# Optimization experiments

Measured on AMD Instinct MI355X. Metric: run time of the kernel, lower is better.

The kernel has to match this reference:

```python
import jax, jax.numpy as jnp
import numpy as np

# 9 jitter shifts: (L, R, T, B) padding applied to `input`; `target` gets the
# opposite padding (L<->R, T<->B swapped), producing a 1-pixel relative shift.
SHIFTS = ((0, 0, 0, 0), (0, 0, 1, 0), (0, 0, 0, 1), (1, 0, 0, 0), (0, 1, 0, 0),
          (1, 0, 1, 0), (0, 1, 0, 1), (0, 1, 1, 0), (1, 0, 0, 1))
SMIN_K = 32.0


def _shifted_diff(inp, tgt, L, R, T, B):
    # get_opposite in the original simply swaps the pad pair
    Lt, Rt = R, L
    Tt, Bt = B, T
    # ConstantPad2d((L,R,T,B)) pads last dim by (L,R), second-to-last by (T,B)
    pi = jnp.pad(inp, ((0, 0), (T, B), (L, R)))
    pt = jnp.pad(tgt, ((0, 0), (Tt, Bt), (Lt, Rt)))  # same padded shape
    d = jnp.abs(pi - pt)
    n, m, k = d.shape
    # crop back to the original (batch, max_len, dim) window
    return d[:, T:m - B, L:k - R]


def setup_inputs() -> dict:
    key = jax.random.key(0)
    k1, k2 = jax.random.split(key)
    B, T, D = 64, 2048, 80
    return {
        "input": jax.random.normal(k1, (B, T, D), dtype=jnp.float32),
        "target": jax.random.normal(k2, (B, T, D), dtype=jnp.float32),
    }


def reference(input, target):
    # (batch, max_len, dim, 9): abs-diff for each of the 9 relative shifts
    diffs = jnp.stack(
        [_shifted_diff(input, target, L, R, T, B) for (L, R, T, B) in SHIFTS],
        axis=-1,
    )
    # smooth minimum over the 9 shifts: -log(sum(exp(-k*t)))/k (stable via logsumexp)
    sm = -jax.scipy.special.logsumexp(-SMIN_K * diffs, axis=-1) / SMIN_K
    center = diffs[..., 0]  # unshifted abs-diff
    # average of the center diff and the smooth-min, reduced to a scalar loss
    return 0.5 * (jnp.mean(center) + jnp.mean(sm))
```

## Files before the change

### kernel.cpp

```cpp
#include <hip/hip_runtime.h>
#include <math.h>

#define BATCH 64
#define TLEN 2048
#define DIM 80
#define DQ (DIM / 4)
#define TT 8
#define TCHUNKS (TLEN / TT)
#define THREADS 256
#define NSTRIPS (BATCH * TCHUNKS * DQ)
#define NBLOCKS (NSTRIPS / THREADS)

#define SMIN_C  46.166241308446828f
#define SMIN_RC 0.02166084939249829f

__device__ __forceinline__ void load_row(float r[6], const float* __restrict__ base,
                                         int t, int q) {
    if (t >= 0 && t < TLEN) {
        const float* p = base + (size_t)t * DIM;
        const float4 v = *(const float4*)p;
        r[0] = (q > 0)      ? p[-1] : 0.f;
        r[1] = v.x; r[2] = v.y; r[3] = v.z; r[4] = v.w;
        r[5] = (q < DQ - 1) ? p[4]  : 0.f;
    } else {
#pragma unroll
        for (int i = 0; i < 6; ++i) r[i] = 0.f;
    }
}

__device__ __forceinline__ float elem_loss(float x, const float* rm, const float* r0,
                                           const float* rp, int e) {
    float v[9];
#pragma unroll
    for (int i = 0; i < 3; ++i) {
        v[0 + i] = fabsf(x - rm[e + i]);
        v[3 + i] = fabsf(x - r0[e + i]);
        v[6 + i] = fabsf(x - rp[e + i]);
    }
    const float center = v[4];
    float m = fminf(fminf(fminf(v[0], v[1]), fminf(v[2], v[3])),
                    fminf(fminf(v[4], v[5]), fminf(v[6], v[7])));
    m = fminf(m, v[8]);
    float S = 0.f;
#pragma unroll
    for (int s = 0; s < 9; ++s)
        S += __builtin_amdgcn_exp2f(SMIN_C * (m - v[s]));
    const float sm = m - __builtin_amdgcn_logf(S) * SMIN_RC;
    return center + sm;
}

__global__ __launch_bounds__(THREADS) void jitter_kernel(
    const float* __restrict__ inp, const float* __restrict__ tgt,
    float* __restrict__ ws)
{
    __shared__ float wsum[THREADS / 64];

    const int n   = blockIdx.x * THREADS + threadIdx.x;
    const int q   = n % DQ;
    const int rem = n / DQ;
    const int tc  = rem % TCHUNKS;
    const int b   = rem / TCHUNKS;
    const int t0  = tc * TT;
    const int d0  = q * 4;

    const float* tgb = tgt + (size_t)b * TLEN * DIM + d0;
    const float* inb = inp + (size_t)b * TLEN * DIM + d0;

    float rm[6], r0[6], rp[6];
    load_row(rm, tgb, t0 - 1, q);
    load_row(r0, tgb, t0,     q);

    float acc = 0.f;
#pragma unroll
    for (int lt = 0; lt < TT; ++lt) {
        load_row(rp, tgb, t0 + lt + 1, q);
        const float4 in4 = *(const float4*)(inb + (size_t)(t0 + lt) * DIM);
        acc += elem_loss(in4.x, rm, r0, rp, 0);
        acc += elem_loss(in4.y, rm, r0, rp, 1);
        acc += elem_loss(in4.z, rm, r0, rp, 2);
        acc += elem_loss(in4.w, rm, r0, rp, 3);
#pragma unroll
        for (int i = 0; i < 6; ++i) { rm[i] = r0[i]; r0[i] = rp[i]; }
    }

#pragma unroll
    for (int off = 32; off > 0; off >>= 1)
        acc += __shfl_down(acc, off, 64);
    const int lane = threadIdx.x & 63, wid = threadIdx.x >> 6;
    if (lane == 0) wsum[wid] = acc;
    __syncthreads();
    if (threadIdx.x == 0) {
        float tot = 0.f;
#pragma unroll
        for (int w = 0; w < THREADS / 64; ++w) tot += wsum[w];
        ws[blockIdx.x] = tot;
    }
}

__global__ __launch_bounds__(256) void reduce_kernel(const float* __restrict__ ws,
                                                     float* __restrict__ out) {
    __shared__ float wsum[4];
    float s = 0.f;
    for (int i = threadIdx.x; i < NBLOCKS; i += 256) s += ws[i];
#pragma unroll
    for (int off = 32; off > 0; off >>= 1)
        s += __shfl_down(s, off, 64);
    const int lane = threadIdx.x & 63, wid = threadIdx.x >> 6;
    if (lane == 0) wsum[wid] = s;
    __syncthreads();
    if (threadIdx.x == 0) {
        float tot = wsum[0] + wsum[1] + wsum[2] + wsum[3];
        out[0] = tot * (0.5f / (float)((size_t)BATCH * TLEN * DIM));
    }
}

extern "C" void kernel_launch(void* const* d_in, const int* in_sizes, int n_in,
                              void* d_out, int out_size, void* d_ws, size_t ws_size,
                              hipStream_t stream) {
    const float* inp = (const float*)d_in[0];
    const float* tgt = (const float*)d_in[1];
    float* ws  = (float*)d_ws;
    float* out = (float*)d_out;

    jitter_kernel<<<NBLOCKS, THREADS, 0, stream>>>(inp, tgt, ws);
    reduce_kernel<<<1, 256, 0, stream>>>(ws, out);
}
```

Baseline: 112.1 us.

## Fuse final reduction via atomics, fold exp argument into FMA, add occupancy hint

The separate reduce kernel is replaced by per-block atomicAdd into a global accumulator. A last-block-done counter writes the final scaled loss, and a tiny zero kernel resets the accumulator before the main kernel. The exp2 argument is rewritten as a single FMA using a precomputed scaled minimum, and launch_bounds gains a minimum-blocks hint of 6. The float atomic accumulation makes the summation order nondeterministic, and the zero kernel is still a second launch.

```diff
diff --git a/kernel.cpp b/kernel.cpp
--- a/kernel.cpp
+++ b/kernel.cpp
@@ -41,17 +41,18 @@
     float m = fminf(fminf(fminf(v[0], v[1]), fminf(v[2], v[3])),
                     fminf(fminf(v[4], v[5]), fminf(v[6], v[7])));
     m = fminf(m, v[8]);
+    const float cm = SMIN_C * m;
     float S = 0.f;
 #pragma unroll
     for (int s = 0; s < 9; ++s)
-        S += __builtin_amdgcn_exp2f(SMIN_C * (m - v[s]));
+        S += __builtin_amdgcn_exp2f(fmaf(-SMIN_C, v[s], cm));
     const float sm = m - __builtin_amdgcn_logf(S) * SMIN_RC;
     return center + sm;
 }
 
-__global__ __launch_bounds__(THREADS) void jitter_kernel(
+__global__ __launch_bounds__(THREADS, 6) void jitter_kernel(
     const float* __restrict__ inp, const float* __restrict__ tgt,
-    float* __restrict__ ws)
+    float* __restrict__ ws, float* __restrict__ out)
 {
     __shared__ float wsum[THREADS / 64];
 
@@ -93,25 +94,19 @@
         float tot = 0.f;
 #pragma unroll
         for (int w = 0; w < THREADS / 64; ++w) tot += wsum[w];
-        ws[blockIdx.x] = tot;
+        atomicAdd(&ws[0], tot);
+        __threadfence();
+        int old = atomicAdd((int*)ws + 1, 1);
+        if (old == NBLOCKS - 1) {
+            __threadfence();
+            const float s = atomicAdd(&ws[0], 0.f);
+            out[0] = s * (0.5f / (float)((size_t)BATCH * TLEN * DIM));
+        }
     }
 }
 
-__global__ __launch_bounds__(256) void reduce_kernel(const float* __restrict__ ws,
-                                                     float* __restrict__ out) {
-    __shared__ float wsum[4];
-    float s = 0.f;
-    for (int i = threadIdx.x; i < NBLOCKS; i += 256) s += ws[i];
-#pragma unroll
-    for (int off = 32; off > 0; off >>= 1)
-        s += __shfl_down(s, off, 64);
-    const int lane = threadIdx.x & 63, wid = threadIdx.x >> 6;
-    if (lane == 0) wsum[wid] = s;
-    __syncthreads();
-    if (threadIdx.x == 0) {
-        float tot = wsum[0] + wsum[1] + wsum[2] + wsum[3];
-        out[0] = tot * (0.5f / (float)((size_t)BATCH * TLEN * DIM));
-    }
+__global__ void zero_kernel(float* ws) {
+    if (threadIdx.x < 2) ws[threadIdx.x] = 0.f;
 }
 
 extern "C" void kernel_launch(void* const* d_in, const int* in_sizes, int n_in,
@@ -122,6 +117,6 @@
     float* ws  = (float*)d_ws;
     float* out = (float*)d_out;
 
-    jitter_kernel<<<NBLOCKS, THREADS, 0, stream>>>(inp, tgt, ws);
-    reduce_kernel<<<1, 256, 0, stream>>>(ws, out);
+    zero_kernel<<<1, 64, 0, stream>>>(ws);
+    jitter_kernel<<<NBLOCKS, THREADS, 0, stream>>>(inp, tgt, ws, out);
 }
```

Measured after the change: 162.5 us. 45.0% more time.
